# Optimization experiments

Hardware: AMD Instinct MI355X
Metric: run time of the kernel (lower is better)

The kernel has to match this reference:

```python
import jax, jax.numpy as jnp
import numpy as np

MIN_NORM = 1e-15
BALL_EPS = 4e-3  # float32 eps used by hgcn PoincareBall.proj
C = 1.0          # curvature


def _artanh(x):
    return jnp.arctanh(jnp.clip(x, -1.0 + 1e-7, 1.0 - 1e-7))


def _norm(x):
    return jnp.clip(jnp.linalg.norm(x, axis=-1, keepdims=True), MIN_NORM)


def proj(x, c):
    n = _norm(x)
    maxn = (1.0 - BALL_EPS) / jnp.sqrt(c)
    return jnp.where(n > maxn, x / n * maxn, x)


def expmap0(u, c):
    sq = jnp.sqrt(c)
    un = _norm(u)
    return jnp.tanh(sq * un) * u / (sq * un)


def logmap0(p, c):
    sq = jnp.sqrt(c)
    pn = _norm(p)
    return _artanh(sq * pn) * p / (sq * pn)


def mobius_add(x, y, c):
    x2 = jnp.sum(x * x, -1, keepdims=True)
    y2 = jnp.sum(y * y, -1, keepdims=True)
    xy = jnp.sum(x * y, -1, keepdims=True)
    num = (1.0 + 2.0 * c * xy + c * y2) * x + (1.0 - c * x2) * y
    den = 1.0 + 2.0 * c * xy + c * c * x2 * y2
    return num / jnp.clip(den, MIN_NORM)


def mobius_matvec(m, x, c):
    sq = jnp.sqrt(c)
    xn = _norm(x)
    mx = x @ m.T  # [N, out]
    mxn = _norm(mx)
    res = jnp.tanh(mxn / xn * _artanh(sq * xn)) * mx / (mxn * sq)
    cond = jnp.all(mx == 0, axis=-1, keepdims=True)
    return jnp.where(cond, jnp.zeros_like(res), res)


def setup_inputs() -> dict:
    key = jax.random.key(0)
    N, D, K, E, DEG = 100000, 512, 16, 3200000, 32
    k1, k2, k3, k4, k5, k6 = jax.random.split(key, 6)
    # valid points on the Poincare ball: expmap0 of small tangent vectors
    x_t = 0.1 * jax.random.normal(k1, (N, D), dtype=jnp.float32)
    x = proj(expmap0(x_t, C), C)
    weight = jax.random.normal(k2, (K, D), dtype=jnp.float32) / np.sqrt(D)
    bias = 0.01 * jax.random.normal(k3, (K,), dtype=jnp.float32)
    # sparse normalized adjacency as edge list
    edge_src = jax.random.randint(k4, (E,), 0, N, dtype=jnp.int64)
    edge_dst = jax.random.randint(k5, (E,), 0, N, dtype=jnp.int64)
    edge_w = jax.random.uniform(k6, (E,), dtype=jnp.float32) / DEG
    return {"x": x, "weight": weight, "bias": bias, "edge_w": edge_w,
            "edge_src": edge_src, "edge_dst": edge_dst}


def reference(x, weight, bias, edge_w, edge_src, edge_dst):
    c = jnp.float32(C)
    n_nodes = x.shape[0]
    # --- HypLinear (dropout=0) ---
    mv = proj(mobius_matvec(weight, x, c), c)                 # [N, K]
    hyp_bias = proj(expmap0(bias[None, :], c), c)             # [1, K]
    h = proj(mobius_add(mv, hyp_bias, c), c)
    # --- HypAgg: aggregate in tangent space at origin via sparse adj ---
    xt = logmap0(h, c)                                        # [N, K]
    msg = edge_w[:, None] * xt[edge_src]                      # [E, K]
    agg = jax.ops.segment_sum(msg, edge_dst, num_segments=n_nodes)
    h = proj(expmap0(agg, c), c)
    # --- HypAct (act = identity, c_in = c_out = c; proj_tan0 is identity) ---
    xt2 = logmap0(h, c)
    h = proj(expmap0(xt2, c), c)
    # --- decode: proj_tan0(logmap0(x, c), c); proj_tan0 identity on the ball ---
    return logmap0(h, c)
```

## Files before the change

### kernel.cpp

```cpp
#include <hip/hip_runtime.h>
#include <math.h>

#define MIN_NORM 1e-15f
#define MAXN     0.996f
#define ATC      0.9999999f

__device__ __forceinline__ float fast_artanh(float v) {
    v = fminf(fmaxf(v, -ATC), ATC);
    return 0.5f * __logf((1.0f + v) / (1.0f - v));
}
__device__ __forceinline__ float fast_tanh(float xv) {
    float e2 = __expf(2.0f * xv);
    return (e2 - 1.0f) / (e2 + 1.0f);
}
__device__ __forceinline__ float reduce16(float v) {
    v += __shfl_xor(v, 1);
    v += __shfl_xor(v, 2);
    v += __shfl_xor(v, 4);
    v += __shfl_xor(v, 8);
    return v;
}

__global__ __launch_bounds__(256) void hgcn_k1(
    const float* __restrict__ x, const float* __restrict__ weight,
    const float* __restrict__ bias, float* __restrict__ xt, int N)
{
    const int tid  = threadIdx.x;
    const int lane = tid & 63;
    const int wib  = tid >> 6;
    const int k    = lane & 15;

    float wr[16][8];
    const float* wp = weight + lane * 8;
#pragma unroll
    for (int kk = 0; kk < 16; ++kk) {
        float4 a = *(const float4*)(wp + kk * 512);
        float4 b = *(const float4*)(wp + kk * 512 + 4);
        wr[kk][0] = a.x; wr[kk][1] = a.y; wr[kk][2] = a.z; wr[kk][3] = a.w;
        wr[kk][4] = b.x; wr[kk][5] = b.y; wr[kk][6] = b.z; wr[kk][7] = b.w;
    }

    float bb = bias[k];
    float b2 = reduce16(bb * bb);
    float bn = fmaxf(sqrtf(b2), MIN_NORM);
    float eb = fast_tanh(bn) * bb / bn;
    float e2 = reduce16(eb * eb);
    float en = fmaxf(sqrtf(e2), MIN_NORM);
    float hb = (en > MAXN) ? eb * (MAXN / en) : eb;
    float y2 = reduce16(hb * hb);

    const long long wstride = (long long)gridDim.x * 4;
    long long row = (long long)blockIdx.x * 4 + wib;

    float4 c0, c1;
    if (row < N) {
        const float* xr = x + row * 512 + lane * 8;
        c0 = *(const float4*)(xr);
        c1 = *(const float4*)(xr + 4);
    }

    while (row < N) {
        long long nrow = row + wstride;
        float4 n0, n1;
        if (nrow < N) {
            const float* xr = x + nrow * 512 + lane * 8;
            n0 = *(const float4*)(xr);
            n1 = *(const float4*)(xr + 4);
        }

        float xv[8] = {c0.x, c0.y, c0.z, c0.w, c1.x, c1.y, c1.z, c1.w};

        float p = 0.0f;
#pragma unroll
        for (int jj = 0; jj < 8; ++jj) p = fmaf(xv[jj], xv[jj], p);
#pragma unroll
        for (int m = 1; m <= 32; m <<= 1) p += __shfl_xor(p, m);
        const float x2 = p;

        float acc[16];
#pragma unroll
        for (int kk = 0; kk < 16; ++kk) {
            float s = 0.0f;
#pragma unroll
            for (int jj = 0; jj < 8; ++jj) s = fmaf(wr[kk][jj], xv[jj], s);
            acc[kk] = s;
        }

        float v8[8];
        {
            const bool h = lane & 1;
#pragma unroll
            for (int i = 0; i < 8; ++i) {
                float keep = h ? acc[2*i+1] : acc[2*i];
                float give = h ? acc[2*i]   : acc[2*i+1];
                v8[i] = keep + __shfl_xor(give, 1);
            }
        }
        float v4[4];
        {
            const bool h = lane & 2;
#pragma unroll
            for (int i = 0; i < 4; ++i) {
                float keep = h ? v8[2*i+1] : v8[2*i];
                float give = h ? v8[2*i]   : v8[2*i+1];
                v4[i] = keep + __shfl_xor(give, 2);
            }
        }
        float v2[2];
        {
            const bool h = lane & 4;
#pragma unroll
            for (int i = 0; i < 2; ++i) {
                float keep = h ? v4[2*i+1] : v4[2*i];
                float give = h ? v4[2*i]   : v4[2*i+1];
                v2[i] = keep + __shfl_xor(give, 4);
            }
        }
        float mx;
        {
            const bool h = lane & 8;
            float keep = h ? v2[1] : v2[0];
            float give = h ? v2[0] : v2[1];
            mx = keep + __shfl_xor(give, 8);
        }
        mx += __shfl_xor(mx, 16);
        mx += __shfl_xor(mx, 32);

        float mx2 = reduce16(mx * mx);
        float xn  = fmaxf(sqrtf(x2),  MIN_NORM);
        float mxn = fmaxf(sqrtf(mx2), MIN_NORM);
        float res = fast_tanh(mxn / xn * fast_artanh(xn)) * mx / mxn;
        if (mx2 == 0.0f) res = 0.0f;
        float rn2 = reduce16(res * res);
        float rn  = fmaxf(sqrtf(rn2), MIN_NORM);
        float mv  = (rn > MAXN) ? res * (MAXN / rn) : res;
        float mv2 = reduce16(mv * mv);
        float xy  = reduce16(mv * hb);
        float num = (1.0f + 2.0f * xy + y2) * mv + (1.0f - mv2) * hb;
        float den = 1.0f + 2.0f * xy + mv2 * y2;
        float hq  = num / fmaxf(den, MIN_NORM);
        float hn2 = reduce16(hq * hq);
        float hn  = fmaxf(sqrtf(hn2), MIN_NORM);
        float hp  = (hn > MAXN) ? hq * (MAXN / hn) : hq;
        float hp2 = reduce16(hp * hp);
        float pn  = fmaxf(sqrtf(hp2), MIN_NORM);
        float xtv = fast_artanh(pn) * hp / pn;

        if (lane < 16) xt[row * 16 + lane] = xtv;

        c0 = n0; c1 = n1;
        row = nrow;
    }
}

__global__ void hgcn_k_detect(const void* srcp, long long E, int* flag)
{
    const int tid = threadIdx.x;
    if (tid == 0) *flag = 0;
    __syncthreads();
    long long n = E / 2; if (n > 4096) n = 4096;
    int bad = 0;
    const unsigned long long* p = (const unsigned long long*)srcp;
    for (long long i = tid; i < n; i += 256)
        if (p[i] >= (1ULL << 32)) bad = 1;
    if (bad) atomicOr(flag, 1);
}

__global__ __launch_bounds__(256) void hgcn_k2(
    const void* __restrict__ srcp, const void* __restrict__ dstp,
    const float* __restrict__ ew, const float* __restrict__ xt,
    float* __restrict__ agg, long long E, const int* __restrict__ flag)
{
    long long gid = (long long)blockIdx.x * 256 + threadIdx.x;
    long long e = gid >> 4;
    int k = (int)(gid & 15);
    if (e >= E) return;
    long long s, d;
    if (*flag) {
        s = ((const int*)srcp)[e];
        d = ((const int*)dstp)[e];
    } else {
        s = ((const long long*)srcp)[e];
        d = ((const long long*)dstp)[e];
    }
    float w = ew[e];
    atomicAdd(&agg[d * 16 + k], w * xt[s * 16 + k]);
}

__global__ __launch_bounds__(256) void hgcn_k3(float* __restrict__ out, int N)
{
    int gid = blockIdx.x * blockDim.x + threadIdx.x;
    int row = gid >> 4;
    if (row >= N) return;
    float u = out[(size_t)row * 16 + (gid & 15)];

    float un2 = reduce16(u * u);
    float un  = fmaxf(sqrtf(un2), MIN_NORM);
    float h1  = fast_tanh(un) * u / un;
    float n2  = reduce16(h1 * h1);
    float n1  = fmaxf(sqrtf(n2), MIN_NORM);
    float h1p = (n1 > MAXN) ? h1 * (MAXN / n1) : h1;
    float m2  = reduce16(h1p * h1p);
    float pn  = fmaxf(sqrtf(m2), MIN_NORM);
    float xt2 = fast_artanh(pn) * h1p / pn;
    float a2  = reduce16(xt2 * xt2);
    float an  = fmaxf(sqrtf(a2), MIN_NORM);
    float h2  = fast_tanh(an) * xt2 / an;
    float b2  = reduce16(h2 * h2);
    float bn  = fmaxf(sqrtf(b2), MIN_NORM);
    float h2p = (bn > MAXN) ? h2 * (MAXN / bn) : h2;
    float c2  = reduce16(h2p * h2p);
    float cn  = fmaxf(sqrtf(c2), MIN_NORM);
    out[(size_t)row * 16 + (gid & 15)] = fast_artanh(cn) * h2p / cn;
}

extern "C" void kernel_launch(void* const* d_in, const int* in_sizes, int n_in,
                              void* d_out, int out_size, void* d_ws, size_t ws_size,
                              hipStream_t stream)
{
    const float* x        = (const float*)d_in[0];
    const float* weight   = (const float*)d_in[1];
    const float* bias     = (const float*)d_in[2];
    const float* edge_w   = (const float*)d_in[3];
    const void*  edge_src = d_in[4];
    const void*  edge_dst = d_in[5];

    const int Kv = in_sizes[2];
    const int Dv = in_sizes[1] / Kv;
    const int N  = in_sizes[0] / Dv;
    const long long E = in_sizes[3];

    int*   flag = (int*)d_ws;
    float* xt   = (float*)((char*)d_ws + 256);
    float* agg  = (float*)d_out;

    hipMemsetAsync(d_out, 0, (size_t)N * 16 * sizeof(float), stream);
    hipLaunchKernelGGL(hgcn_k_detect, dim3(1), dim3(256), 0, stream, edge_src, E, flag);
    hipLaunchKernelGGL(hgcn_k1, dim3(1024), dim3(256), 0, stream,
                       x, weight, bias, xt, N);
    long long thr = E * 16;
    hipLaunchKernelGGL(hgcn_k2, dim3((unsigned)((thr + 255) / 256)), dim3(256), 0, stream,
                       edge_src, edge_dst, edge_w, xt, agg, E, flag);
    hipLaunchKernelGGL(hgcn_k3, dim3((unsigned)(((long long)N * 16 + 255) / 256)), dim3(256), 0, stream,
                       agg, N);
}
```

Measured before the change: 311.3 us.

## Batch four rows per wave in linear kernel and grid-stride the edge scatter

The linear kernel now has each wave process four consecutive rows per iteration. Each 16-lane group keeps one row's matvec result, so the long serial chain of mobius and norm reductions runs once per four rows instead of once per row, and more lanes do useful work in the epilogue. The edge scatter kernel becomes a fixed 2048-block grid-stride loop that prefetches the next edge's indices, weight and gathered value before issuing the current atomic add. This cuts launch size and hides gather latency, but limits parallelism to the fixed grid and adds register pressure in the first kernel.

```diff
diff --git a/kernel.cpp b/kernel.cpp
--- a/kernel.cpp
+++ b/kernel.cpp
@@ -29,6 +29,7 @@
     const int lane = tid & 63;
     const int wib  = tid >> 6;
     const int k    = lane & 15;
+    const int grp  = lane >> 4;
 
     float wr[16][8];
     const float* wp = weight + lane * 8;
@@ -49,87 +50,92 @@
     float hb = (en > MAXN) ? eb * (MAXN / en) : eb;
     float y2 = reduce16(hb * hb);
 
-    const long long wstride = (long long)gridDim.x * 4;
-    long long row = (long long)blockIdx.x * 4 + wib;
-
-    float4 c0, c1;
-    if (row < N) {
-        const float* xr = x + row * 512 + lane * 8;
+    const long long stride = (long long)gridDim.x * 4 * 4;
+    long long base = ((long long)blockIdx.x * 4 + wib) * 4;
+
+    float4 c0 = {0,0,0,0}, c1 = {0,0,0,0};
+    if (base < N) {
+        const float* xr = x + base * 512 + lane * 8;
         c0 = *(const float4*)(xr);
         c1 = *(const float4*)(xr + 4);
     }
 
-    while (row < N) {
-        long long nrow = row + wstride;
-        float4 n0, n1;
-        if (nrow < N) {
-            const float* xr = x + nrow * 512 + lane * 8;
-            n0 = *(const float4*)(xr);
-            n1 = *(const float4*)(xr + 4);
+    while (base < N) {
+        float x2sel = 0.0f, mxsel = 0.0f;
+
+#pragma unroll
+        for (int p = 0; p < 4; ++p) {
+            long long nrow = (p < 3) ? (base + p + 1) : (base + stride);
+            float4 n0 = {0,0,0,0}, n1 = {0,0,0,0};
+            if (nrow < N) {
+                const float* xr = x + nrow * 512 + lane * 8;
+                n0 = *(const float4*)(xr);
+                n1 = *(const float4*)(xr + 4);
+            }
+
+            float xv[8] = {c0.x, c0.y, c0.z, c0.w, c1.x, c1.y, c1.z, c1.w};
+
+            float pq = 0.0f;
+#pragma unroll
+            for (int jj = 0; jj < 8; ++jj) pq = fmaf(xv[jj], xv[jj], pq);
+#pragma unroll
+            for (int m = 1; m <= 32; m <<= 1) pq += __shfl_xor(pq, m);
+            if (grp == p) x2sel = pq;
+
+            float v8[8];
+            {
+                const bool h = lane & 1;
+#pragma unroll
+                for (int i = 0; i < 8; ++i) {
+                    float a0 = 0.0f, a1 = 0.0f;
+#pragma unroll
+                    for (int jj = 0; jj < 8; ++jj) {
+                        a0 = fmaf(wr[2*i][jj],   xv[jj], a0);
+                        a1 = fmaf(wr[2*i+1][jj], xv[jj], a1);
+                    }
+                    float keep = h ? a1 : a0;
+                    float give = h ? a0 : a1;
+                    v8[i] = keep + __shfl_xor(give, 1);
+                }
+            }
+            float v4[4];
+            {
+                const bool h = lane & 2;
+#pragma unroll
+                for (int i = 0; i < 4; ++i) {
+                    float keep = h ? v8[2*i+1] : v8[2*i];
+                    float give = h ? v8[2*i]   : v8[2*i+1];
+                    v4[i] = keep + __shfl_xor(give, 2);
+                }
+            }
+            float v2[2];
+            {
+                const bool h = lane & 4;
+#pragma unroll
+                for (int i = 0; i < 2; ++i) {
+                    float keep = h ? v4[2*i+1] : v4[2*i];
+                    float give = h ? v4[2*i]   : v4[2*i+1];
+                    v2[i] = keep + __shfl_xor(give, 4);
+                }
+            }
+            float mx;
+            {
+                const bool h = lane & 8;
+                float keep = h ? v2[1] : v2[0];
+                float give = h ? v2[0] : v2[1];
+                mx = keep + __shfl_xor(give, 8);
+            }
+            mx += __shfl_xor(mx, 16);
+            mx += __shfl_xor(mx, 32);
+            if (grp == p) mxsel = mx;
+
+            c0 = n0; c1 = n1;
         }
 
-        float xv[8] = {c0.x, c0.y, c0.z, c0.w, c1.x, c1.y, c1.z, c1.w};
-
-        float p = 0.0f;
-#pragma unroll
-        for (int jj = 0; jj < 8; ++jj) p = fmaf(xv[jj], xv[jj], p);
-#pragma unroll
-        for (int m = 1; m <= 32; m <<= 1) p += __shfl_xor(p, m);
-        const float x2 = p;
-
-        float acc[16];
-#pragma unroll
-        for (int kk = 0; kk < 16; ++kk) {
-            float s = 0.0f;
-#pragma unroll
-            for (int jj = 0; jj < 8; ++jj) s = fmaf(wr[kk][jj], xv[jj], s);
-            acc[kk] = s;
-        }
-
-        float v8[8];
-        {
-            const bool h = lane & 1;
-#pragma unroll
-            for (int i = 0; i < 8; ++i) {
-                float keep = h ? acc[2*i+1] : acc[2*i];
-                float give = h ? acc[2*i]   : acc[2*i+1];
-                v8[i] = keep + __shfl_xor(give, 1);
-            }
-        }
-        float v4[4];
-        {
-            const bool h = lane & 2;
-#pragma unroll
-            for (int i = 0; i < 4; ++i) {
-                float keep = h ? v8[2*i+1] : v8[2*i];
-                float give = h ? v8[2*i]   : v8[2*i+1];
-                v4[i] = keep + __shfl_xor(give, 2);
-            }
-        }
-        float v2[2];
-        {
-            const bool h = lane & 4;
-#pragma unroll
-            for (int i = 0; i < 2; ++i) {
-                float keep = h ? v4[2*i+1] : v4[2*i];
-                float give = h ? v4[2*i]   : v4[2*i+1];
-                v2[i] = keep + __shfl_xor(give, 4);
-            }
-        }
-        float mx;
-        {
-            const bool h = lane & 8;
-            float keep = h ? v2[1] : v2[0];
-            float give = h ? v2[0] : v2[1];
-            mx = keep + __shfl_xor(give, 8);
-        }
-        mx += __shfl_xor(mx, 16);
-        mx += __shfl_xor(mx, 32);
-
-        float mx2 = reduce16(mx * mx);
-        float xn  = fmaxf(sqrtf(x2),  MIN_NORM);
-        float mxn = fmaxf(sqrtf(mx2), MIN_NORM);
-        float res = fast_tanh(mxn / xn * fast_artanh(xn)) * mx / mxn;
+        float mx2 = reduce16(mxsel * mxsel);
+        float xn  = fmaxf(sqrtf(x2sel), MIN_NORM);
+        float mxn = fmaxf(sqrtf(mx2),   MIN_NORM);
+        float res = fast_tanh(mxn / xn * fast_artanh(xn)) * mxsel / mxn;
         if (mx2 == 0.0f) res = 0.0f;
         float rn2 = reduce16(res * res);
         float rn  = fmaxf(sqrtf(rn2), MIN_NORM);
@@ -146,10 +152,10 @@
         float pn  = fmaxf(sqrtf(hp2), MIN_NORM);
         float xtv = fast_artanh(pn) * hp / pn;
 
-        if (lane < 16) xt[row * 16 + lane] = xtv;
-
-        c0 = n0; c1 = n1;
-        row = nrow;
+        long long myrow = base + grp;
+        if (myrow < N) xt[myrow * 16 + k] = xtv;
+
+        base += stride;
     }
 }
 
@@ -171,20 +177,34 @@
     const float* __restrict__ ew, const float* __restrict__ xt,
     float* __restrict__ agg, long long E, const int* __restrict__ flag)
 {
-    long long gid = (long long)blockIdx.x * 256 + threadIdx.x;
-    long long e = gid >> 4;
-    int k = (int)(gid & 15);
-    if (e >= E) return;
-    long long s, d;
-    if (*flag) {
-        s = ((const int*)srcp)[e];
-        d = ((const int*)dstp)[e];
-    } else {
-        s = ((const long long*)srcp)[e];
-        d = ((const long long*)dstp)[e];
-    }
-    float w = ew[e];
-    atomicAdd(&agg[d * 16 + k], w * xt[s * 16 + k]);
+    const int k = threadIdx.x & 15;
+    const bool i32 = (*flag != 0);
+    const long long slots = ((long long)gridDim.x * 256) >> 4;
+    long long e = ((long long)blockIdx.x * 256 + threadIdx.x) >> 4;
+
+    long long d0 = 0; float w0 = 0.0f, v0 = 0.0f;
+    bool have = e < E;
+    if (have) {
+        long long s0;
+        if (i32) { s0 = ((const int*)srcp)[e];       d0 = ((const int*)dstp)[e]; }
+        else     { s0 = ((const long long*)srcp)[e]; d0 = ((const long long*)dstp)[e]; }
+        w0 = ew[e];
+        v0 = xt[s0 * 16 + k];
+    }
+    while (have) {
+        long long en = e + slots;
+        long long d1 = 0; float w1 = 0.0f, v1 = 0.0f;
+        bool haven = en < E;
+        if (haven) {
+            long long s1;
+            if (i32) { s1 = ((const int*)srcp)[en];       d1 = ((const int*)dstp)[en]; }
+            else     { s1 = ((const long long*)srcp)[en]; d1 = ((const long long*)dstp)[en]; }
+            w1 = ew[en];
+            v1 = xt[s1 * 16 + k];
+        }
+        atomicAdd(&agg[d0 * 16 + k], w0 * v0);
+        e = en; d0 = d1; w0 = w1; v0 = v1; have = haven;
+    }
 }
 
 __global__ __launch_bounds__(256) void hgcn_k3(float* __restrict__ out, int N)
@@ -238,8 +258,7 @@
     hipLaunchKernelGGL(hgcn_k_detect, dim3(1), dim3(256), 0, stream, edge_src, E, flag);
     hipLaunchKernelGGL(hgcn_k1, dim3(1024), dim3(256), 0, stream,
                        x, weight, bias, xt, N);
-    long long thr = E * 16;
-    hipLaunchKernelGGL(hgcn_k2, dim3((unsigned)((thr + 255) / 256)), dim3(256), 0, stream,
+    hipLaunchKernelGGL(hgcn_k2, dim3(2048), dim3(256), 0, stream,
                        edge_src, edge_dst, edge_w, xt, agg, E, flag);
     hipLaunchKernelGGL(hgcn_k3, dim3((unsigned)(((long long)N * 16 + 255) / 256)), dim3(256), 0, stream,
                        agg, N);
```

Result: faster. 257.4 us (-17.3%).
